# Kernel optimization log

Measured on AMD Instinct MI355X. Metric: run time of the kernel, lower is better.

The kernel has to match this reference:

```python
import jax, jax.numpy as jnp
import numpy as np

N = 1_000_000      # total atoms
B = 1024           # number of molecules (batch segments)
NUM_ELEMENTS = 118
D_EMB = 64
D_HID = 128


def setup_inputs() -> dict:
    key = jax.random.key(0)
    ks = jax.random.split(key, 9)
    positions = jax.random.normal(ks[0], (N, 3), dtype=jnp.float32) * 5.0
    atomic_numbers = jax.random.randint(ks[1], (N,), 0, NUM_ELEMENTS, dtype=jnp.int64)
    batch = jnp.sort(jax.random.randint(ks[2], (N,), 0, B, dtype=jnp.int64))
    # learned parameters (torch Linear is y = x @ W.T + b; we store W as (in, out))
    embed = jax.random.normal(ks[3], (NUM_ELEMENTS, D_EMB), dtype=jnp.float32) * 0.1
    W1 = jax.random.normal(ks[4], (D_EMB, D_HID), dtype=jnp.float32) * (1.0 / np.sqrt(D_EMB))
    b1 = jnp.zeros((D_HID,), dtype=jnp.float32)
    W2 = jax.random.normal(ks[5], (D_HID, D_HID), dtype=jnp.float32) * (1.0 / np.sqrt(D_HID))
    b2 = jnp.zeros((D_HID,), dtype=jnp.float32)
    W3 = jax.random.normal(ks[6], (D_HID, 1), dtype=jnp.float32) * (1.0 / np.sqrt(D_HID))
    b3 = jnp.zeros((1,), dtype=jnp.float32)
    return {
        "positions": positions,
        "embed": embed,
        "W1": W1, "b1": b1,
        "W2": W2, "b2": b2,
        "W3": W3, "b3": b3,
        "atomic_numbers": atomic_numbers,
        "batch": batch,
    }


def reference(positions, embed, W1, b1, W2, b2, W3, b3, atomic_numbers, batch):
    def energy_fn(pos):
        h = embed[atomic_numbers]                       # [N, 64] gather
        pos_feat = jnp.sum(pos, axis=-1, keepdims=True) # [N, 1]
        h = h + 0.0 * pos_feat                          # keeps pos in the graph (grad is zero)
        x = jax.nn.silu(h @ W1 + b1)                    # [N, 128]
        x = jax.nn.silu(x @ W2 + b2)                    # [N, 128]
        per_atom = (x @ W3 + b3)[:, 0]                  # [N]
        # energy.scatter_add_(0, batch, per_atom)
        return jax.ops.segment_sum(per_atom, batch, num_segments=B)  # [B]

    energy = energy_fn(positions)
    # forces = -grad_R sum(V(R)); identically zero here but computed faithfully
    forces = -jax.grad(lambda p: energy_fn(p).sum())(positions)      # [N, 3]
    return (energy, forces)
```

## Files before the change

### kernel.cpp

```cpp
#include <hip/hip_runtime.h>

#define D_EMB   64
#define D_HID   128
#define NUM_EL  118

__global__ void mace_etab_kernel(const float* __restrict__ embed,
                                 const float* __restrict__ W1, const float* __restrict__ b1,
                                 const float* __restrict__ W2, const float* __restrict__ b2,
                                 const float* __restrict__ W3, const float* __restrict__ b3,
                                 float* __restrict__ Etab) {
    __shared__ float h[D_EMB];
    __shared__ float x1[D_HID];
    __shared__ float wsum[2];
    const int z = blockIdx.x;
    const int t = threadIdx.x;

    if (t < D_EMB) h[t] = embed[z * D_EMB + t];
    __syncthreads();

    float acc = b1[t];
    #pragma unroll
    for (int k = 0; k < D_EMB; ++k)
        acc = fmaf(h[k], W1[k * D_HID + t], acc);
    x1[t] = acc / (1.0f + expf(-acc));
    __syncthreads();

    float acc2 = b2[t];
    #pragma unroll
    for (int k = 0; k < D_HID; ++k)
        acc2 = fmaf(x1[k], W2[k * D_HID + t], acc2);
    float s2 = acc2 / (1.0f + expf(-acc2));
    float r = s2 * W3[t];

    #pragma unroll
    for (int off = 32; off > 0; off >>= 1)
        r += __shfl_down(r, off, 64);
    if ((t & 63) == 0) wsum[t >> 6] = r;
    __syncthreads();
    if (t == 0) Etab[z] = wsum[0] + wsum[1] + b3[0];
}

__device__ __forceinline__ int lower_bound_wave(const int* __restrict__ arr,
                                                int n, int target) {
    int lo = 0, hi = n;
    const int lane = threadIdx.x & 63;
    while (hi > lo) {
        const int range = hi - lo;
        const int step  = (range + 63) >> 6;
        const int pos   = lo + lane * step;
        const bool lt   = (pos < hi) && (arr[pos] < target);
        const unsigned long long m = __ballot(lt);
        const int k = __popcll(m);
        if (k == 0) { hi = lo; break; }
        const int new_lo = lo + (k - 1) * step + 1;
        int new_hi = lo + k * step;
        if (new_hi > hi) new_hi = hi;
        lo = new_lo; hi = new_hi;
    }
    return lo;
}

__global__ __launch_bounds__(256)
void mace_segsum_kernel(const int* __restrict__ z,
                        const int* __restrict__ batch,
                        const float* __restrict__ EtabG,
                        float* __restrict__ energy,
                        float4* __restrict__ forces4,
                        int n, int nf4) {
    __shared__ float etab_s[NUM_EL];
    __shared__ int   bounds[2];
    __shared__ float wsum[4];
    const int b = blockIdx.x;
    const int t = threadIdx.x;
    const int w = t >> 6;

    if (t < NUM_EL) etab_s[t] = EtabG[t];

    const int gstride = gridDim.x * blockDim.x;
    for (int i = b * blockDim.x + t; i < nf4; i += gstride)
        forces4[i] = make_float4(0.f, 0.f, 0.f, 0.f);

    if (w == 0) {
        const int s = lower_bound_wave(batch, n, b);
        if ((t & 63) == 0) bounds[0] = s;
    } else if (w == 1) {
        const int e = lower_bound_wave(batch, n, b + 1);
        if ((t & 63) == 0) bounds[1] = e;
    }
    __syncthreads();

    const int start = bounds[0], end = bounds[1];
    float acc = 0.f;
    for (int i = start + t; i < end; i += 256)
        acc += etab_s[z[i]];

    #pragma unroll
    for (int off = 32; off > 0; off >>= 1)
        acc += __shfl_down(acc, off, 64);
    if ((t & 63) == 0) wsum[w] = acc;
    __syncthreads();
    if (t == 0) energy[b] = wsum[0] + wsum[1] + wsum[2] + wsum[3];
}

extern "C" void kernel_launch(void* const* d_in, const int* in_sizes, int n_in,
                              void* d_out, int out_size, void* d_ws, size_t ws_size,
                              hipStream_t stream) {
    const float* embed = (const float*)d_in[1];
    const float* W1    = (const float*)d_in[2];
    const float* b1    = (const float*)d_in[3];
    const float* W2    = (const float*)d_in[4];
    const float* b2    = (const float*)d_in[5];
    const float* W3    = (const float*)d_in[6];
    const float* b3    = (const float*)d_in[7];
    const int*   z     = (const int*)d_in[8];
    const int*   batch = (const int*)d_in[9];
    const int    n     = in_sizes[8];

    const int B   = out_size - 3 * n;
    const int nf4 = (3 * n) / 4;

    float*  energy  = (float*)d_out;
    float4* forces4 = (float4*)((float*)d_out + B);
    float*  Etab    = (float*)d_ws;

    mace_etab_kernel<<<NUM_EL, D_HID, 0, stream>>>(embed, W1, b1, W2, b2, W3, b3, Etab);
    mace_segsum_kernel<<<B, 256, 0, stream>>>(z, batch, Etab, energy, forces4, n, nf4);
}
```

Baseline: 15.03 us.

## Move force zeroing into the table kernel and vectorize atomic-number loads

The zero-fill of the forces buffer moves from the segment-sum kernel into the first kernel, now launched with 2048 blocks of 256 threads, and the first 118 blocks also compute the per-element energy table. The aim is to overlap the memory-bound zeroing with the small MLP work. The segment-sum loop now reads atomic numbers as int4 with scalar head and tail handling, which cuts load instructions, and the MLP dot products use four independent accumulators to shorten FMA dependency chains. In exchange, the first kernel is larger, and half the threads in the table blocks sit idle.

```diff
diff --git a/kernel.cpp b/kernel.cpp
--- a/kernel.cpp
+++ b/kernel.cpp
@@ -3,41 +3,65 @@
 #define D_EMB   64
 #define D_HID   128
 #define NUM_EL  118
+#define PREP_GRID 2048
 
-__global__ void mace_etab_kernel(const float* __restrict__ embed,
-                                 const float* __restrict__ W1, const float* __restrict__ b1,
-                                 const float* __restrict__ W2, const float* __restrict__ b2,
-                                 const float* __restrict__ W3, const float* __restrict__ b3,
-                                 float* __restrict__ Etab) {
-    __shared__ float h[D_EMB];
-    __shared__ float x1[D_HID];
-    __shared__ float wsum[2];
-    const int z = blockIdx.x;
+__global__ __launch_bounds__(256)
+void mace_prep_kernel(const float* __restrict__ embed,
+                      const float* __restrict__ W1, const float* __restrict__ b1,
+                      const float* __restrict__ W2, const float* __restrict__ b2,
+                      const float* __restrict__ W3, const float* __restrict__ b3,
+                      float* __restrict__ Etab,
+                      float4* __restrict__ forces4, int nf4) {
     const int t = threadIdx.x;
 
-    if (t < D_EMB) h[t] = embed[z * D_EMB + t];
-    __syncthreads();
+    const int gstride = gridDim.x * blockDim.x;
+    for (int i = blockIdx.x * blockDim.x + t; i < nf4; i += gstride)
+        forces4[i] = make_float4(0.f, 0.f, 0.f, 0.f);
 
-    float acc = b1[t];
-    #pragma unroll
-    for (int k = 0; k < D_EMB; ++k)
-        acc = fmaf(h[k], W1[k * D_HID + t], acc);
-    x1[t] = acc / (1.0f + expf(-acc));
-    __syncthreads();
+    if (blockIdx.x < NUM_EL) {
+        __shared__ float h[D_EMB];
+        __shared__ float x1[D_HID];
+        __shared__ float wsum[2];
+        const int z = blockIdx.x;
 
-    float acc2 = b2[t];
-    #pragma unroll
-    for (int k = 0; k < D_HID; ++k)
-        acc2 = fmaf(x1[k], W2[k * D_HID + t], acc2);
-    float s2 = acc2 / (1.0f + expf(-acc2));
-    float r = s2 * W3[t];
+        if (t < D_EMB) h[t] = embed[z * D_EMB + t];
+        __syncthreads();
 
-    #pragma unroll
-    for (int off = 32; off > 0; off >>= 1)
-        r += __shfl_down(r, off, 64);
-    if ((t & 63) == 0) wsum[t >> 6] = r;
-    __syncthreads();
-    if (t == 0) Etab[z] = wsum[0] + wsum[1] + b3[0];
+        if (t < D_HID) {
+            float a0 = 0.f, a1 = 0.f, a2 = 0.f, a3 = 0.f;
+            #pragma unroll
+            for (int k = 0; k < D_EMB; k += 4) {
+                a0 = fmaf(h[k + 0], W1[(k + 0) * D_HID + t], a0);
+                a1 = fmaf(h[k + 1], W1[(k + 1) * D_HID + t], a1);
+                a2 = fmaf(h[k + 2], W1[(k + 2) * D_HID + t], a2);
+                a3 = fmaf(h[k + 3], W1[(k + 3) * D_HID + t], a3);
+            }
+            const float acc = b1[t] + ((a0 + a1) + (a2 + a3));
+            x1[t] = acc / (1.0f + expf(-acc));
+        }
+        __syncthreads();
+
+        float r = 0.f;
+        if (t < D_HID) {
+            float a0 = 0.f, a1 = 0.f, a2 = 0.f, a3 = 0.f;
+            #pragma unroll
+            for (int k = 0; k < D_HID; k += 4) {
+                a0 = fmaf(x1[k + 0], W2[(k + 0) * D_HID + t], a0);
+                a1 = fmaf(x1[k + 1], W2[(k + 1) * D_HID + t], a1);
+                a2 = fmaf(x1[k + 2], W2[(k + 2) * D_HID + t], a2);
+                a3 = fmaf(x1[k + 3], W2[(k + 3) * D_HID + t], a3);
+            }
+            const float acc2 = b2[t] + ((a0 + a1) + (a2 + a3));
+            const float s2 = acc2 / (1.0f + expf(-acc2));
+            r = s2 * W3[t];
+        }
+        #pragma unroll
+        for (int off = 32; off > 0; off >>= 1)
+            r += __shfl_down(r, off, 64);
+        if (t < D_HID && (t & 63) == 0) wsum[t >> 6] = r;
+        __syncthreads();
+        if (t == 0) Etab[z] = wsum[0] + wsum[1] + b3[0];
+    }
 }
 
 __device__ __forceinline__ int lower_bound_wave(const int* __restrict__ arr,
@@ -64,9 +88,7 @@
 void mace_segsum_kernel(const int* __restrict__ z,
                         const int* __restrict__ batch,
                         const float* __restrict__ EtabG,
-                        float* __restrict__ energy,
-                        float4* __restrict__ forces4,
-                        int n, int nf4) {
+                        float* __restrict__ energy, int n) {
     __shared__ float etab_s[NUM_EL];
     __shared__ int   bounds[2];
     __shared__ float wsum[4];
@@ -75,10 +97,6 @@
     const int w = t >> 6;
 
     if (t < NUM_EL) etab_s[t] = EtabG[t];
-
-    const int gstride = gridDim.x * blockDim.x;
-    for (int i = b * blockDim.x + t; i < nf4; i += gstride)
-        forces4[i] = make_float4(0.f, 0.f, 0.f, 0.f);
 
     if (w == 0) {
         const int s = lower_bound_wave(batch, n, b);
@@ -91,8 +109,18 @@
 
     const int start = bounds[0], end = bounds[1];
     float acc = 0.f;
-    for (int i = start + t; i < end; i += 256)
-        acc += etab_s[z[i]];
+
+    int a0 = (start + 3) & ~3;
+    if (a0 > end) a0 = end;
+    const int a1 = (end >= a0) ? (end & ~3) : a0;
+
+    if (t < a0 - start) acc += etab_s[z[start + t]];
+    if (a1 >= a0 && t < end - a1) acc += etab_s[z[a1 + t]];
+    const int4* __restrict__ z4 = (const int4*)z;
+    for (int i4 = (a0 >> 2) + t; i4 < (a1 >> 2); i4 += 256) {
+        const int4 v = z4[i4];
+        acc += etab_s[v.x] + etab_s[v.y] + etab_s[v.z] + etab_s[v.w];
+    }
 
     #pragma unroll
     for (int off = 32; off > 0; off >>= 1)
@@ -123,6 +151,7 @@
     float4* forces4 = (float4*)((float*)d_out + B);
     float*  Etab    = (float*)d_ws;
 
-    mace_etab_kernel<<<NUM_EL, D_HID, 0, stream>>>(embed, W1, b1, W2, b2, W3, b3, Etab);
-    mace_segsum_kernel<<<B, 256, 0, stream>>>(z, batch, Etab, energy, forces4, n, nf4);
+    mace_prep_kernel<<<PREP_GRID, 256, 0, stream>>>(embed, W1, b1, W2, b2, W3, b3,
+                                                    Etab, forces4, nf4);
+    mace_segsum_kernel<<<B, 256, 0, stream>>>(z, batch, Etab, energy, n);
 }
```

Result: faster. 14.64 us (-2.6%).
